# Optimization experiments

Hardware: AMD Instinct MI355X
Metric: run time of the kernel (lower is better)

The kernel has to match this reference:

```python
import jax, jax.numpy as jnp
import numpy as np

FREQ = 4
EXP_DIM = 32
INTERP_LEVEL = 3
DEFORM_SCALE = 0.1
BBOX = ((0.0, 1.0), (0.0, 1.0), (0.0, 1.0))
B, N = 2, 262144


def embed(x):
    # positional embedding: [x, sin(2^k x), cos(2^k x)] k=0..FREQ-1 (include_input, log sampling)
    feats = [x]
    for k in range(FREQ):
        s = x * (2.0 ** k)
        feats.append(jnp.sin(s))
        feats.append(jnp.cos(s))
    return jnp.concatenate(feats, axis=-1)


def mlp(x, W1, b1, W2, b2):
    return jax.nn.relu(x @ W1 + b1) @ W2 + b2


def grid_sample3d(vol, grid):
    # vol [C,D,H,W], grid [N,3] with (x,y,z) in [-1,1]; trilinear, align_corners=False, zero padding
    C, D, H, W = vol.shape
    fx = ((grid[:, 0] + 1.0) * W - 1.0) * 0.5
    fy = ((grid[:, 1] + 1.0) * H - 1.0) * 0.5
    fz = ((grid[:, 2] + 1.0) * D - 1.0) * 0.5
    x0 = jnp.floor(fx); y0 = jnp.floor(fy); z0 = jnp.floor(fz)
    wx = fx - x0; wy = fy - y0; wz = fz - z0
    x0i = x0.astype(jnp.int32); y0i = y0.astype(jnp.int32); z0i = z0.astype(jnp.int32)

    def gather(zi, yi, xi):
        valid = ((zi >= 0) & (zi < D) & (yi >= 0) & (yi < H) & (xi >= 0) & (xi < W))
        zc = jnp.clip(zi, 0, D - 1); yc = jnp.clip(yi, 0, H - 1); xc = jnp.clip(xi, 0, W - 1)
        return vol[:, zc, yc, xc] * valid.astype(vol.dtype)[None, :]

    out = jnp.zeros((C, grid.shape[0]), vol.dtype)
    for dz in (0, 1):
        for dy in (0, 1):
            for dx in (0, 1):
                w = ((wz if dz else 1.0 - wz) * (wy if dy else 1.0 - wy) * (wx if dx else 1.0 - wx))
                out = out + gather(z0i + dz, y0i + dy, x0i + dx) * w[None, :]
    return out


def normalize_pts(pts, bbox):
    # pts [B,3,N] -> grid [B,N,3] in [-1,1]
    uvw = []
    for i in range(3):
        lo, hi = bbox[i]
        uvw.append((pts[:, i] - 0.5 * (lo + hi)) / (0.5 * (hi - lo)))
    return jnp.stack(uvw, axis=-1)


def mult_dist_interp(pts, vol, bbox):
    # pts [B,3,N], vol [B,C,D,H,W] -> [B, C*INTERP_LEVEL, N]
    grid = normalize_pts(pts, bbox)
    feats = []
    for i in range(INTERP_LEVEL):
        s = 2 ** i
        sub = vol[:, :, ::s, ::s, ::s]
        feats.append(jax.vmap(grid_sample3d)(sub, grid))
    return jnp.concatenate(feats, axis=1)


def bcn_to_nc(x):
    b, c, n = x.shape
    return x.transpose(0, 2, 1).reshape(b * n, c)


def nc_to_bcn(x, b):
    bn, c = x.shape
    return x.reshape(b, bn // b, c).transpose(0, 2, 1)


def setup_inputs() -> dict:
    key = jax.random.key(0)
    ks = jax.random.split(key, 20)
    d = {
        'query_pts': jax.random.uniform(ks[0], (B, 3, N), jnp.float32),
        'query_viewdirs': jax.random.normal(ks[1], (B, 3, N), jnp.float32),
        'exp': jax.random.normal(ks[2], (B, 32), jnp.float32),
        'deform_bs_volume': jax.random.normal(ks[3], (32, 4, 32, 32, 32), jnp.float32) * 0.1,
        'deform_mean_volume': jax.random.normal(ks[4], (4, 32, 32, 32), jnp.float32) * 0.1,
        'feature_volume': jax.random.normal(ks[5], (8, 64, 64, 64), jnp.float32) * 0.1,
        'dW1': jax.random.normal(ks[6], (108, 64), jnp.float32) * 0.1,
        'db1': jnp.zeros((64,), jnp.float32),
        'dW2': jax.random.normal(ks[7], (64, 3), jnp.float32) * 0.1,
        'db2': jnp.zeros((3,), jnp.float32),
        'sW1': jax.random.normal(ks[8], (248, 128), jnp.float32) * 0.06,
        'sb1': jnp.zeros((128,), jnp.float32),
        'sW2': jax.random.normal(ks[9], (128, 1), jnp.float32) * 0.1,
        'sb2': jnp.zeros((1,), jnp.float32),
        'cW1': jax.random.normal(ks[10], (275, 128), jnp.float32) * 0.06,
        'cb1': jnp.zeros((128,), jnp.float32),
        'cW2': jax.random.normal(ks[11], (128, 3), jnp.float32) * 0.1,
        'cb2': jnp.zeros((3,), jnp.float32),
    }
    return d


def reference(query_pts, query_viewdirs, exp, deform_bs_volume, deform_mean_volume,
              feature_volume, dW1, db1, dW2, db2, sW1, sb1, sW2, sb2, cW1, cb1, cW2, cb2):
    b = query_pts.shape[0]
    exp_c = exp[:, :EXP_DIM]
    # deform volume: exp-blendshape combination  [B, Cd, R, R, R]
    deform_vol = jnp.einsum('be,ecdhw->bcdhw', exp_c, deform_bs_volume) + deform_mean_volume[None]
    deform = mult_dist_interp(query_pts, deform_vol, BBOX)            # [B, 12, N]
    offset = nc_to_bcn(mlp(embed(bcn_to_nc(deform)), dW1, db1, dW2, db2), b)  # [B,3,N]
    deformed_pts = offset * DEFORM_SCALE + query_pts
    fvol = jnp.broadcast_to(feature_volume[None], (b,) + feature_volume.shape)
    feature = mult_dist_interp(deformed_pts, fvol, BBOX)              # [B, 24, N]
    fe = embed(bcn_to_nc(feature))                                    # [(B N), 216]
    ve = embed(bcn_to_nc(query_viewdirs))                             # [(B N), 27]
    n = query_pts.shape[2]
    exp_n = jnp.broadcast_to((exp_c / 3.0)[:, None, :], (b, n, EXP_DIM)).reshape(b * n, EXP_DIM)
    density = nc_to_bcn(mlp(jnp.concatenate([fe, exp_n], 1), sW1, sb1, sW2, sb2), b)  # [B,1,N]
    color = jax.nn.sigmoid(nc_to_bcn(mlp(jnp.concatenate([fe, ve, exp_n], 1), cW1, cb1, cW2, cb2), b))  # [B,3,N]
    return offset, density, color
```

## Files before the change

### kernel.cpp

```cpp
#include <hip/hip_runtime.h>
#include <math.h>

#define NPTS 262144
#define RSTR 66

typedef __attribute__((ext_vector_type(4))) float f32x4;
typedef __attribute__((ext_vector_type(8))) short s16x8;

__device__ __forceinline__ unsigned short f2bf(float f) {
    union { float f; unsigned u; } v; v.f = f;
    unsigned u = v.u;
    return (unsigned short)((u + 0x7fffu + ((u >> 16) & 1u)) >> 16);
}
__device__ __forceinline__ float bf2f(unsigned short h) {
    union { unsigned u; float f; } v; v.u = ((unsigned)h) << 16;
    return v.f;
}
__device__ __forceinline__ unsigned rnd16(float f) {
    union { float f; unsigned u; } v; v.f = f;
    return v.u + 0x7fffu + ((v.u >> 16) & 1u);
}
__device__ __forceinline__ unsigned packbf(float lo, float hi) {
#if defined(__has_builtin)
#if __has_builtin(__builtin_amdgcn_perm)
    return __builtin_amdgcn_perm(rnd16(hi), rnd16(lo), 0x07060302u);
#else
    return (rnd16(hi) & 0xffff0000u) | (rnd16(lo) >> 16);
#endif
#else
    return (rnd16(hi) & 0xffff0000u) | (rnd16(lo) >> 16);
#endif
}

__device__ __forceinline__ int swz(int e) {
    return e ^ (((e >> 7) & 1) << 3) ^ (((e >> 8) & 1) << 4);
}

__device__ __forceinline__ int XF(int kt, int mt, int lane) {
    return ((kt * 4 + mt) * 64 + lane) * 8;
}

__device__ __forceinline__ int fragAddr(int p, int k) {
    int kt = k >> 5, kk = k & 31;
    int lane = (((kk & 15) >> 2) << 4) | (p & 15);
    int j = ((kk >> 4) << 2) | (kk & 3);
    int mt = (p >> 4) & 3;
    return swz((((kt * 4 + mt) * 64) + lane) * 8 + j);
}

__global__ void k_deform_vol_t(const float* __restrict__ exp_,
                               const float* __restrict__ bs,
                               const float* __restrict__ mean,
                               float* __restrict__ dvt) {
    int idx = blockIdx.x * blockDim.x + threadIdx.x;
    int c = idx & 3;
    int v = (idx >> 2) & 32767;
    int b = idx >> 17;
    float acc = mean[c * 32768 + v];
    #pragma unroll 8
    for (int e = 0; e < 32; ++e)
        acc = fmaf(exp_[b * 32 + e], bs[(e * 4 + c) * 32768 + v], acc);
    dvt[idx] = acc;
}

__global__ void k_ftr(const float* __restrict__ fvol, float* __restrict__ fvt) {
    int i = blockIdx.x * blockDim.x + threadIdx.x;
    int c = i >> 18;
    int v = i & 262143;
    fvt[v * 8 + c] = fvol[i];
}

__global__ void k_hb(const float* __restrict__ exp_,
                     const float* __restrict__ sW1, const float* __restrict__ sb1,
                     const float* __restrict__ cW1, const float* __restrict__ cb1,
                     float* __restrict__ sHb, float* __restrict__ cHb) {
    int b = blockIdx.x;
    int j = threadIdx.x;
    float a = sb1[j];
    float a2 = cb1[j];
    for (int e = 0; e < 32; ++e) {
        float ev = exp_[b * 32 + e] * (1.0f / 3.0f);
        a  = fmaf(ev, sW1[(216 + e) * 128 + j], a);
        a2 = fmaf(ev, cW1[(243 + e) * 128 + j], a2);
    }
    sHb[b * 128 + j] = a;
    cHb[b * 128 + j] = a2;
}

__global__ void k_wprep(const float* __restrict__ src,
                        unsigned short* __restrict__ dhi,
                        unsigned short* __restrict__ dlo,
                        int KT, int Nsrc, int Ksrc, int mode, int total) {
    int i = blockIdx.x * 256 + threadIdx.x;
    if (i >= total) return;
    int j = i & 7, lane = (i >> 3) & 63;
    int tile = i >> 9;
    int kt = tile % KT, nt = tile / KT;
    int n = nt * 16 + (lane & 15);
    int k = kt * 32 + ((lane >> 4) << 2) + (j & 3) + ((j >> 2) << 4);
    int row = -1;
    if (mode == 0) {
        row = (k < Ksrc) ? k : -1;
    } else if (mode == 1) {
        int g = k >> 5, tg = (k >> 4) & 1, r = k & 15;
        if (r < 12) row = 12 + 24 * g + 12 * tg + r;
        else { int idx = (2 * g + tg) * 4 + (r - 12); row = (idx < 12) ? idx : -1; }
    } else {
        int g = k >> 6, tg = (k >> 5) & 1, r = k & 31;
        if (r < 24) row = 24 + 48 * g + 24 * tg + r;
        else if (r < 27) row = (mode == 3) ? 219 + 6 * g + 3 * tg + (r - 24) : -1;
        else {
            int idx = (2 * g + tg) * 5 + (r - 27);
            if (idx < 24) row = idx;
            else if (idx < 27 && mode == 3) row = 216 + (idx - 24);
            else row = -1;
        }
    }
    float v = (row >= 0 && n < Nsrc) ? src[row * Nsrc + n] : 0.0f;
    unsigned short h = f2bf(v);
    dhi[i] = h;
    if (dlo) dlo[i] = f2bf(v - bf2f(h));
}

template<int S, int STEP, int DIM, int NC>
__device__ __forceinline__ void lerp_cl(const float* __restrict__ vol,
                                        float px, float py, float pz,
                                        float* __restrict__ o) {
    float fx = px * (float)S - 0.5f;
    float fy = py * (float)S - 0.5f;
    float fz = pz * (float)S - 0.5f;
    float x0 = floorf(fx), y0 = floorf(fy), z0 = floorf(fz);
    float wx = fx - x0, wy = fy - y0, wz = fz - z0;
    int ix = (int)x0, iy = (int)y0, iz = (int)z0;
    #pragma unroll
    for (int c = 0; c < NC; ++c) o[c] = 0.0f;
    #pragma unroll
    for (int dz = 0; dz < 2; ++dz)
    #pragma unroll
    for (int dy = 0; dy < 2; ++dy)
    #pragma unroll
    for (int dx = 0; dx < 2; ++dx) {
        int xi = ix + dx, yi = iy + dy, zi = iz + dz;
        bool valid = (xi >= 0) & (xi < S) & (yi >= 0) & (yi < S) & (zi >= 0) & (zi < S);
        int xc = min(max(xi, 0), S - 1);
        int yc = min(max(yi, 0), S - 1);
        int zc = min(max(zi, 0), S - 1);
        float w = (dz ? wz : 1.f - wz) * (dy ? wy : 1.f - wy) * (dx ? wx : 1.f - wx);
        w = valid ? w : 0.f;
        const float4* q = (const float4*)(vol +
            (size_t)(((zc * STEP) * DIM + yc * STEP) * DIM + xc * STEP) * NC);
        float4 v0 = q[0];
        o[0] = fmaf(v0.x, w, o[0]); o[1] = fmaf(v0.y, w, o[1]);
        o[2] = fmaf(v0.z, w, o[2]); o[3] = fmaf(v0.w, w, o[3]);
        if (NC == 8) {
            float4 v1 = q[1];
            o[4] = fmaf(v1.x, w, o[4]); o[5] = fmaf(v1.y, w, o[5]);
            o[6] = fmaf(v1.z, w, o[6]); o[7] = fmaf(v1.w, w, o[7]);
        }
    }
}

template<int C, int BD, int S, int STEP>
__device__ __forceinline__ void trilerp_cm(const float* __restrict__ vol,
                                           float px, float py, float pz,
                                           float* __restrict__ out) {
    float fx = px * (float)S - 0.5f;
    float fy = py * (float)S - 0.5f;
    float fz = pz * (float)S - 0.5f;
    float x0 = floorf(fx), y0 = floorf(fy), z0 = floorf(fz);
    float wx = fx - x0, wy = fy - y0, wz = fz - z0;
    int ix = (int)x0, iy = (int)y0, iz = (int)z0;
    #pragma unroll
    for (int c = 0; c < C; ++c) out[c] = 0.0f;
    #pragma unroll
    for (int dz = 0; dz < 2; ++dz)
    #pragma unroll
    for (int dy = 0; dy < 2; ++dy)
    #pragma unroll
    for (int dx = 0; dx < 2; ++dx) {
        int xi = ix + dx, yi = iy + dy, zi = iz + dz;
        bool valid = (xi >= 0) & (xi < S) & (yi >= 0) & (yi < S) & (zi >= 0) & (zi < S);
        int xc = min(max(xi, 0), S - 1);
        int yc = min(max(yi, 0), S - 1);
        int zc = min(max(zi, 0), S - 1);
        float w = (dz ? wz : 1.f - wz) * (dy ? wy : 1.f - wy) * (dx ? wx : 1.f - wx);
        w = valid ? w : 0.f;
        int off = ((zc * STEP) * BD + yc * STEP) * BD + xc * STEP;
        #pragma unroll
        for (int c = 0; c < C; ++c)
            out[c] = fmaf(vol[c * (BD * BD * BD) + off], w, out[c]);
    }
}

#define MFMA(a, b, c) __builtin_amdgcn_mfma_f32_16x16x32_bf16((a), (b), (c), 0, 0, 0)

template<bool CL>
__global__ __launch_bounds__(256, 4) void k_main(
    const float* __restrict__ qp, const float* __restrict__ qv,
    const float* __restrict__ dvt, const float* __restrict__ fvol,
    const float* __restrict__ db1, const float* __restrict__ db2,
    const float* __restrict__ sb2, const float* __restrict__ cb2,
    const float* __restrict__ sHb, const float* __restrict__ cHb,
    const unsigned short* __restrict__ dW1h, const unsigned short* __restrict__ dW1l,
    const unsigned short* __restrict__ sW1h,
    const unsigned short* __restrict__ cW1f,
    const unsigned short* __restrict__ dW2f, const unsigned short* __restrict__ sW2f,
    const unsigned short* __restrict__ cW2f,
    float* __restrict__ out)
{
    __shared__ __align__(16) unsigned short xfrag[16384];
    __shared__ __align__(16) float raw[28 * RSTR];
    __shared__ float dp[3 * 64];

    const int t = threadIdx.x;
    const int lane = t & 63;
    const int w = t >> 6;
    const int gp0 = blockIdx.x * 64;
    const int b = gp0 / NPTS;
    const int n0 = gp0 - b * NPTS;
    const float* qpb = qp + b * 3 * NPTS;
    const float* qvb = qv + b * 3 * NPTS;

    const int cc = (lane >> 4) << 2;
    const int pp = w * 16 + (lane & 15);

    {
        const float* dv = dvt + b * 131072;
        if (t < 192) {
            int p = t & 63, lvl = t >> 6;
            int n = n0 + p;
            float px = qpb[n], py = qpb[NPTS + n], pz = qpb[2 * NPTS + n];
            float o[4];
            if (lvl == 0)      lerp_cl<32, 1, 32, 4>(dv, px, py, pz, o);
            else if (lvl == 1) lerp_cl<16, 2, 32, 4>(dv, px, py, pz, o);
            else               lerp_cl< 8, 4, 32, 4>(dv, px, py, pz, o);
            #pragma unroll
            for (int c = 0; c < 4; ++c) raw[(lvl * 4 + c) * RSTR + p] = o[c];
        }
        if (t < 64) raw[12 * RSTR + t] = 0.f;
    }
    __syncthreads();

    {
        float s0[4], c0[4];
        #pragma unroll
        for (int m = 0; m < 4; ++m) {
            float x = raw[min(cc + m, 12) * RSTR + pp];
            s0[m] = __sinf(x);
            c0[m] = __cosf(x);
        }
        #pragma unroll
        for (int g = 0; g < 4; ++g) {
            float vs[8];
            #pragma unroll
            for (int m = 0; m < 4; ++m) {
                int r = cc + m;
                bool lad = r < 12;
                int i0 = (2 * g) * 4 + (r - 12);
                int i1 = (2 * g + 1) * 4 + (r - 12);
                float r0 = raw[min(max(i0, 0), 12) * RSTR + pp];
                float r1 = raw[min(max(i1, 0), 12) * RSTR + pp];
                vs[m]     = lad ? s0[m] : r0;
                vs[4 + m] = lad ? c0[m] : r1;
            }
            union { unsigned u[4]; s16x8 v; } pk;
            pk.u[0] = packbf(vs[0], vs[1]);
            pk.u[1] = packbf(vs[2], vs[3]);
            pk.u[2] = packbf(vs[4], vs[5]);
            pk.u[3] = packbf(vs[6], vs[7]);
            *(s16x8*)&xfrag[swz(XF(g, w, lane))] = pk.v;
            if (g < 3) {
                #pragma unroll
                for (int m = 0; m < 4; ++m) {
                    float s2 = 2.f * s0[m] * c0[m];
                    float c2 = c0[m] * c0[m] - s0[m] * s0[m];
                    s0[m] = s2; c0[m] = c2;
                }
            }
        }
    }
    __syncthreads();

    {
        f32x4 acc[4];
        float bias = db1[w * 16 + (lane & 15)];
        #pragma unroll
        for (int mt = 0; mt < 4; ++mt) acc[mt] = (f32x4){bias, bias, bias, bias};
        #pragma unroll 1
        for (int kt = 0; kt < 4; ++kt) {
            s16x8 bh = *(const s16x8*)&dW1h[((w * 4 + kt) * 64 + lane) * 8];
            s16x8 bl = *(const s16x8*)&dW1l[((w * 4 + kt) * 64 + lane) * 8];
            #pragma unroll
            for (int mt = 0; mt < 4; ++mt) {
                s16x8 a = *(const s16x8*)&xfrag[swz(XF(kt, mt, lane))];
                acc[mt] = MFMA(a, bh, acc[mt]);
                acc[mt] = MFMA(a, bl, acc[mt]);
            }
        }
        int j = w * 16 + (lane & 15);
        #pragma unroll
        for (int mt = 0; mt < 4; ++mt) {
            int a0 = fragAddr(mt * 16 + cc, 128 + j);
            #pragma unroll
            for (int i = 0; i < 4; ++i)
                xfrag[a0 ^ (8 * i)] = f2bf(fmaxf(acc[mt][i], 0.f));
        }
    }
    __syncthreads();

    {
        f32x4 acc = (f32x4){0, 0, 0, 0};
        #pragma unroll
        for (int kt = 0; kt < 2; ++kt) {
            s16x8 bb = *(const s16x8*)&dW2f[(kt * 64 + lane) * 8];
            s16x8 a = *(const s16x8*)&xfrag[swz(XF(4 + kt, w, lane))];
            acc = MFMA(a, bb, acc);
        }
        int col = lane & 15;
        if (col < 3) {
            #pragma unroll
            for (int i = 0; i < 4; ++i) {
                int p = w * 16 + ((lane >> 4) << 2) + i;
                float v = acc[i] + db2[col];
                out[(b * 3 + col) * NPTS + n0 + p] = v;
                dp[col * 64 + p] = fmaf(v, 0.1f, qpb[col * NPTS + n0 + p]);
            }
        }
    }
    __syncthreads();

    {
        if (t < 192) {
            int p = t & 63, lvl = t >> 6;
            float px = dp[p], py = dp[64 + p], pz = dp[128 + p];
            float o[8];
            if (CL) {
                if (lvl == 0)      lerp_cl<64, 1, 64, 8>(fvol, px, py, pz, o);
                else if (lvl == 1) lerp_cl<32, 2, 64, 8>(fvol, px, py, pz, o);
                else               lerp_cl<16, 4, 64, 8>(fvol, px, py, pz, o);
            } else {
                if (lvl == 0)      trilerp_cm<8, 64, 64, 1>(fvol, px, py, pz, o);
                else if (lvl == 1) trilerp_cm<8, 64, 32, 2>(fvol, px, py, pz, o);
                else               trilerp_cm<8, 64, 16, 4>(fvol, px, py, pz, o);
            }
            #pragma unroll
            for (int c = 0; c < 8; ++c) raw[(lvl * 8 + c) * RSTR + p] = o[c];
        }
        if (t < 64) {
            int n = n0 + t;
            raw[24 * RSTR + t] = qvb[n];
            raw[25 * RSTR + t] = qvb[NPTS + n];
            raw[26 * RSTR + t] = qvb[2 * NPTS + n];
            raw[27 * RSTR + t] = 0.f;
        }
    }
    __syncthreads();

    {
        float sL[4], cL[4], sH[4], cH[4];
        #pragma unroll
        for (int m = 0; m < 4; ++m) {
            float xl = raw[(cc + m) * RSTR + pp];
            sL[m] = __sinf(xl); cL[m] = __cosf(xl);
            float xh = raw[min(16 + cc + m, 27) * RSTR + pp];
            sH[m] = __sinf(xh); cH[m] = __cosf(xh);
        }
        #pragma unroll
        for (int g = 0; g < 4; ++g) {
            #pragma unroll
            for (int tg = 0; tg < 2; ++tg) {
                float vs[8];
                #pragma unroll
                for (int m = 0; m < 4; ++m) {
                    vs[m] = tg ? cL[m] : sL[m];
                    int rh = 16 + cc + m;
                    int idx = (2 * g + tg) * 5 + (rh - 27);
                    float rsv = raw[min(max(idx, 0), 27) * RSTR + pp];
                    float lad = tg ? cH[m] : sH[m];
                    vs[4 + m] = (rh < 27) ? lad : rsv;
                }
                union { unsigned u[4]; s16x8 v; } pk;
                pk.u[0] = packbf(vs[0], vs[1]);
                pk.u[1] = packbf(vs[2], vs[3]);
                pk.u[2] = packbf(vs[4], vs[5]);
                pk.u[3] = packbf(vs[6], vs[7]);
                *(s16x8*)&xfrag[swz(XF(2 * g + tg, w, lane))] = pk.v;
            }
            if (g < 3) {
                #pragma unroll
                for (int m = 0; m < 4; ++m) {
                    float s2 = 2.f * sL[m] * cL[m];
                    float c2 = cL[m] * cL[m] - sL[m] * sL[m];
                    sL[m] = s2; cL[m] = c2;
                    float s3 = 2.f * sH[m] * cH[m];
                    float c3 = cH[m] * cH[m] - sH[m] * sH[m];
                    sH[m] = s3; cH[m] = c3;
                }
            }
        }
    }
    __syncthreads();

    f32x4 accs[4][2], accc[4][2];
    {
        int nl = lane & 15;
        #pragma unroll
        for (int q = 0; q < 2; ++q) {
            float bsv = sHb[b * 128 + (2 * w + q) * 16 + nl];
            float bcv = cHb[b * 128 + (2 * w + q) * 16 + nl];
            #pragma unroll
            for (int mt = 0; mt < 4; ++mt) {
                accs[mt][q] = (f32x4){bsv, bsv, bsv, bsv};
                accc[mt][q] = (f32x4){bcv, bcv, bcv, bcv};
            }
        }
        #pragma unroll 1
        for (int kt = 0; kt < 8; ++kt) {
            s16x8 bh0 = *(const s16x8*)&sW1h[(((2 * w    ) * 8 + kt) * 64 + lane) * 8];
            s16x8 bh1 = *(const s16x8*)&sW1h[(((2 * w + 1) * 8 + kt) * 64 + lane) * 8];
            #pragma unroll
            for (int mt = 0; mt < 4; ++mt) {
                s16x8 a = *(const s16x8*)&xfrag[swz(XF(kt, mt, lane))];
                accs[mt][0] = MFMA(a, bh0, accs[mt][0]);
                accs[mt][1] = MFMA(a, bh1, accs[mt][1]);
            }
        }
        #pragma unroll 1
        for (int kt = 0; kt < 8; ++kt) {
            s16x8 b0 = *(const s16x8*)&cW1f[(((2 * w    ) * 8 + kt) * 64 + lane) * 8];
            s16x8 b1 = *(const s16x8*)&cW1f[(((2 * w + 1) * 8 + kt) * 64 + lane) * 8];
            #pragma unroll
            for (int mt = 0; mt < 4; ++mt) {
                s16x8 a = *(const s16x8*)&xfrag[swz(XF(kt, mt, lane))];
                accc[mt][0] = MFMA(a, b0, accc[mt][0]);
                accc[mt][1] = MFMA(a, b1, accc[mt][1]);
            }
        }
    }
    __syncthreads();

    {
        #pragma unroll
        for (int q = 0; q < 2; ++q) {
            int j = (2 * w + q) * 16 + (lane & 15);
            #pragma unroll
            for (int mt = 0; mt < 4; ++mt) {
                int a0 = fragAddr(mt * 16 + cc, j);
                #pragma unroll
                for (int i = 0; i < 4; ++i) {
                    int ai = a0 ^ (8 * i);
                    xfrag[ai]        = f2bf(fmaxf(accs[mt][q][i], 0.f));
                    xfrag[ai + 8192] = f2bf(fmaxf(accc[mt][q][i], 0.f));
                }
            }
        }
    }
    __syncthreads();

    {
        f32x4 as = (f32x4){0, 0, 0, 0};
        f32x4 ac = (f32x4){0, 0, 0, 0};
        #pragma unroll
        for (int kt = 0; kt < 4; ++kt) {
            s16x8 bsv = *(const s16x8*)&sW2f[(kt * 64 + lane) * 8];
            s16x8 bcv = *(const s16x8*)&cW2f[(kt * 64 + lane) * 8];
            s16x8 a1 = *(const s16x8*)&xfrag[swz(XF(kt, w, lane))];
            s16x8 a2 = *(const s16x8*)&xfrag[swz(XF(4 + kt, w, lane))];
            as = MFMA(a1, bsv, as);
            ac = MFMA(a2, bcv, ac);
        }
        int col = lane & 15;
        #pragma unroll
        for (int i = 0; i < 4; ++i) {
            int p = w * 16 + ((lane >> 4) << 2) + i;
            if (col == 0)
                out[6 * NPTS + b * NPTS + n0 + p] = as[i] + sb2[0];
            if (col < 3) {
                float v = ac[i] + cb2[col];
                out[8 * NPTS + (b * 3 + col) * NPTS + n0 + p] =
                    1.f / (1.f + __expf(-v));
            }
        }
    }
}

extern "C" void kernel_launch(void* const* d_in, const int* in_sizes, int n_in,
                              void* d_out, int out_size, void* d_ws, size_t ws_size,
                              hipStream_t stream) {
    const float* qp   = (const float*)d_in[0];
    const float* qv   = (const float*)d_in[1];
    const float* exp_ = (const float*)d_in[2];
    const float* bs   = (const float*)d_in[3];
    const float* mean = (const float*)d_in[4];
    const float* fvol = (const float*)d_in[5];
    const float* dW1  = (const float*)d_in[6];
    const float* db1  = (const float*)d_in[7];
    const float* dW2  = (const float*)d_in[8];
    const float* db2  = (const float*)d_in[9];
    const float* sW1  = (const float*)d_in[10];
    const float* sb1  = (const float*)d_in[11];
    const float* sW2  = (const float*)d_in[12];
    const float* sb2  = (const float*)d_in[13];
    const float* cW1  = (const float*)d_in[14];
    const float* cb1  = (const float*)d_in[15];
    const float* cW2  = (const float*)d_in[16];
    const float* cb2  = (const float*)d_in[17];

    float* out = (float*)d_out;
    float* ws  = (float*)d_ws;

    float* dvt = ws;
    float* sHb = ws + 262144;
    float* cHb = ws + 262400;
    unsigned short* wb = (unsigned short*)(ws + 262656);
    unsigned short* dW1h  = wb;
    unsigned short* dW1l  = wb + 8192;
    unsigned short* sW1h  = wb + 16384;
    unsigned short* cW1f_ = wb + 49152;
    unsigned short* dW2f  = wb + 81920;
    unsigned short* sW2f  = wb + 82944;
    unsigned short* cW2f  = wb + 84992;
    float* fvt = ws + 262656 + 43520;
    bool cl = ws_size >= (size_t)(306176 + 2097152) * 4;

    k_deform_vol_t<<<1024, 256, 0, stream>>>(exp_, bs, mean, dvt);
    k_hb<<<2, 128, 0, stream>>>(exp_, sW1, sb1, cW1, cb1, sHb, cHb);
    k_wprep<<<32, 256, 0, stream>>>(dW1, dW1h, dW1l, 4, 64, 128, 1, 8192);
    k_wprep<<<128, 256, 0, stream>>>(sW1, sW1h, nullptr, 8, 128, 256, 2, 32768);
    k_wprep<<<128, 256, 0, stream>>>(cW1, cW1f_, nullptr, 8, 128, 256, 3, 32768);
    k_wprep<<<4, 256, 0, stream>>>(dW2, dW2f, nullptr, 2, 3, 64, 0, 1024);
    k_wprep<<<8, 256, 0, stream>>>(sW2, sW2f, nullptr, 4, 1, 128, 0, 2048);
    k_wprep<<<8, 256, 0, stream>>>(cW2, cW2f, nullptr, 4, 3, 128, 0, 2048);

    if (cl) {
        k_ftr<<<2097152 / 256, 256, 0, stream>>>(fvol, fvt);
        k_main<true><<<8192, 256, 0, stream>>>(
            qp, qv, dvt, fvt, db1, db2, sb2, cb2, sHb, cHb,
            dW1h, dW1l, sW1h, cW1f_, dW2f, sW2f, cW2f, out);
    } else {
        k_main<false><<<8192, 256, 0, stream>>>(
            qp, qv, dvt, fvol, db1, db2, sb2, cb2, sHb, cHb,
            dW1h, dW1l, sW1h, cW1f_, dW2f, sW2f, cW2f, out);
    }
}
```

Before: 253.4 us.

## Make each wave own 16 points end-to-end and replace block barriers with wave waits

Reassigns work so each wavefront processes its own 16 points through all stages. Lanes are split by level for the trilinear sampling, and each wave computes all output columns of every MLP GEMM for its M-tile instead of splitting columns across waves. Since no wave reads another wave's LDS data, all __syncthreads are replaced by an lgkmcnt wait with scheduling barriers, removing block-wide barrier stalls. In exchange each wave loads every weight fragment from global/L2, which raises weight traffic fourfold, and the sampling template now takes runtime sizes and shifts instead of compile-time constants.

```diff
diff --git a/kernel.cpp b/kernel.cpp
--- a/kernel.cpp
+++ b/kernel.cpp
@@ -30,6 +30,12 @@
 #else
     return (rnd16(hi) & 0xffff0000u) | (rnd16(lo) >> 16);
 #endif
+}
+
+__device__ __forceinline__ void wave_sync() {
+    __builtin_amdgcn_sched_barrier(0);
+    asm volatile("s_waitcnt lgkmcnt(0)" ::: "memory");
+    __builtin_amdgcn_sched_barrier(0);
 }
 
 __device__ __forceinline__ int swz(int e) {
@@ -122,13 +128,15 @@
     if (dlo) dlo[i] = f2bf(v - bf2f(h));
 }
 
-template<int S, int STEP, int DIM, int NC>
-__device__ __forceinline__ void lerp_cl(const float* __restrict__ vol,
-                                        float px, float py, float pz,
-                                        float* __restrict__ o) {
-    float fx = px * (float)S - 0.5f;
-    float fy = py * (float)S - 0.5f;
-    float fz = pz * (float)S - 0.5f;
+template<int DIM, int NC>
+__device__ __forceinline__ void lerp_cl_rt(const float* __restrict__ vol,
+                                           int S, int lc,
+                                           float px, float py, float pz,
+                                           float* __restrict__ o) {
+    float fS = (float)S;
+    float fx = px * fS - 0.5f;
+    float fy = py * fS - 0.5f;
+    float fz = pz * fS - 0.5f;
     float x0 = floorf(fx), y0 = floorf(fy), z0 = floorf(fz);
     float wx = fx - x0, wy = fy - y0, wz = fz - z0;
     int ix = (int)x0, iy = (int)y0, iz = (int)z0;
@@ -145,33 +153,35 @@
         int xc = min(max(xi, 0), S - 1);
         int yc = min(max(yi, 0), S - 1);
         int zc = min(max(zi, 0), S - 1);
-        float w = (dz ? wz : 1.f - wz) * (dy ? wy : 1.f - wy) * (dx ? wx : 1.f - wx);
-        w = valid ? w : 0.f;
+        float wgt = (dz ? wz : 1.f - wz) * (dy ? wy : 1.f - wy) * (dx ? wx : 1.f - wx);
+        wgt = valid ? wgt : 0.f;
         const float4* q = (const float4*)(vol +
-            (size_t)(((zc * STEP) * DIM + yc * STEP) * DIM + xc * STEP) * NC);
+            (size_t)(((zc << lc) * DIM + (yc << lc)) * DIM + (xc << lc)) * NC);
         float4 v0 = q[0];
-        o[0] = fmaf(v0.x, w, o[0]); o[1] = fmaf(v0.y, w, o[1]);
-        o[2] = fmaf(v0.z, w, o[2]); o[3] = fmaf(v0.w, w, o[3]);
+        o[0] = fmaf(v0.x, wgt, o[0]); o[1] = fmaf(v0.y, wgt, o[1]);
+        o[2] = fmaf(v0.z, wgt, o[2]); o[3] = fmaf(v0.w, wgt, o[3]);
         if (NC == 8) {
             float4 v1 = q[1];
-            o[4] = fmaf(v1.x, w, o[4]); o[5] = fmaf(v1.y, w, o[5]);
-            o[6] = fmaf(v1.z, w, o[6]); o[7] = fmaf(v1.w, w, o[7]);
-        }
-    }
-}
-
-template<int C, int BD, int S, int STEP>
-__device__ __forceinline__ void trilerp_cm(const float* __restrict__ vol,
+            o[4] = fmaf(v1.x, wgt, o[4]); o[5] = fmaf(v1.y, wgt, o[5]);
+            o[6] = fmaf(v1.z, wgt, o[6]); o[7] = fmaf(v1.w, wgt, o[7]);
+        }
+    }
+}
+
+template<int DIM, int NC>
+__device__ __forceinline__ void lerp_cm_rt(const float* __restrict__ vol,
+                                           int S, int lc,
                                            float px, float py, float pz,
-                                           float* __restrict__ out) {
-    float fx = px * (float)S - 0.5f;
-    float fy = py * (float)S - 0.5f;
-    float fz = pz * (float)S - 0.5f;
+                                           float* __restrict__ o) {
+    float fS = (float)S;
+    float fx = px * fS - 0.5f;
+    float fy = py * fS - 0.5f;
+    float fz = pz * fS - 0.5f;
     float x0 = floorf(fx), y0 = floorf(fy), z0 = floorf(fz);
     float wx = fx - x0, wy = fy - y0, wz = fz - z0;
     int ix = (int)x0, iy = (int)y0, iz = (int)z0;
     #pragma unroll
-    for (int c = 0; c < C; ++c) out[c] = 0.0f;
+    for (int c = 0; c < NC; ++c) o[c] = 0.0f;
     #pragma unroll
     for (int dz = 0; dz < 2; ++dz)
     #pragma unroll
@@ -183,12 +193,12 @@
         int xc = min(max(xi, 0), S - 1);
         int yc = min(max(yi, 0), S - 1);
         int zc = min(max(zi, 0), S - 1);
-        float w = (dz ? wz : 1.f - wz) * (dy ? wy : 1.f - wy) * (dx ? wx : 1.f - wx);
-        w = valid ? w : 0.f;
-        int off = ((zc * STEP) * BD + yc * STEP) * BD + xc * STEP;
-        #pragma unroll
-        for (int c = 0; c < C; ++c)
-            out[c] = fmaf(vol[c * (BD * BD * BD) + off], w, out[c]);
+        float wgt = (dz ? wz : 1.f - wz) * (dy ? wy : 1.f - wy) * (dx ? wx : 1.f - wx);
+        wgt = valid ? wgt : 0.f;
+        int off = ((zc << lc) * DIM + (yc << lc)) * DIM + (xc << lc);
+        #pragma unroll
+        for (int c = 0; c < NC; ++c)
+            o[c] = fmaf(vol[c * (DIM * DIM * DIM) + off], wgt, o[c]);
     }
 }
 
@@ -222,24 +232,26 @@
     const float* qvb = qv + b * 3 * NPTS;
 
     const int cc = (lane >> 4) << 2;
-    const int pp = w * 16 + (lane & 15);
+    const int nl = lane & 15;
+    const int pp = w * 16 + nl;
+    const int pl = lane & 15;
+    const int lvl = lane >> 4;
+    const int pg = w * 16 + pl;
 
     {
         const float* dv = dvt + b * 131072;
-        if (t < 192) {
-            int p = t & 63, lvl = t >> 6;
-            int n = n0 + p;
+        if (lvl < 3) {
+            int n = n0 + pg;
             float px = qpb[n], py = qpb[NPTS + n], pz = qpb[2 * NPTS + n];
             float o[4];
-            if (lvl == 0)      lerp_cl<32, 1, 32, 4>(dv, px, py, pz, o);
-            else if (lvl == 1) lerp_cl<16, 2, 32, 4>(dv, px, py, pz, o);
-            else               lerp_cl< 8, 4, 32, 4>(dv, px, py, pz, o);
-            #pragma unroll
-            for (int c = 0; c < 4; ++c) raw[(lvl * 4 + c) * RSTR + p] = o[c];
-        }
-        if (t < 64) raw[12 * RSTR + t] = 0.f;
-    }
-    __syncthreads();
+            lerp_cl_rt<32, 4>(dv, 32 >> lvl, lvl, px, py, pz, o);
+            #pragma unroll
+            for (int c = 0; c < 4; ++c) raw[(lvl * 4 + c) * RSTR + pg] = o[c];
+        } else {
+            raw[12 * RSTR + pg] = 0.f;
+        }
+    }
+    wave_sync();
 
     {
         float s0[4], c0[4];
@@ -279,34 +291,36 @@
             }
         }
     }
-    __syncthreads();
+    wave_sync();
 
     {
         f32x4 acc[4];
-        float bias = db1[w * 16 + (lane & 15)];
-        #pragma unroll
-        for (int mt = 0; mt < 4; ++mt) acc[mt] = (f32x4){bias, bias, bias, bias};
+        #pragma unroll
+        for (int nt = 0; nt < 4; ++nt) {
+            float bias = db1[nt * 16 + nl];
+            acc[nt] = (f32x4){bias, bias, bias, bias};
+        }
         #pragma unroll 1
         for (int kt = 0; kt < 4; ++kt) {
-            s16x8 bh = *(const s16x8*)&dW1h[((w * 4 + kt) * 64 + lane) * 8];
-            s16x8 bl = *(const s16x8*)&dW1l[((w * 4 + kt) * 64 + lane) * 8];
-            #pragma unroll
-            for (int mt = 0; mt < 4; ++mt) {
-                s16x8 a = *(const s16x8*)&xfrag[swz(XF(kt, mt, lane))];
-                acc[mt] = MFMA(a, bh, acc[mt]);
-                acc[mt] = MFMA(a, bl, acc[mt]);
-            }
-        }
-        int j = w * 16 + (lane & 15);
-        #pragma unroll
-        for (int mt = 0; mt < 4; ++mt) {
-            int a0 = fragAddr(mt * 16 + cc, 128 + j);
+            s16x8 a = *(const s16x8*)&xfrag[swz(XF(kt, w, lane))];
+            #pragma unroll
+            for (int nt = 0; nt < 4; ++nt) {
+                s16x8 bh = *(const s16x8*)&dW1h[((nt * 4 + kt) * 64 + lane) * 8];
+                s16x8 bl = *(const s16x8*)&dW1l[((nt * 4 + kt) * 64 + lane) * 8];
+                acc[nt] = MFMA(a, bh, acc[nt]);
+                acc[nt] = MFMA(a, bl, acc[nt]);
+            }
+        }
+        wave_sync();
+        #pragma unroll
+        for (int nt = 0; nt < 4; ++nt) {
+            int a0 = fragAddr(w * 16 + cc, 128 + nt * 16 + nl);
             #pragma unroll
             for (int i = 0; i < 4; ++i)
-                xfrag[a0 ^ (8 * i)] = f2bf(fmaxf(acc[mt][i], 0.f));
-        }
-    }
-    __syncthreads();
+                xfrag[a0 ^ (8 * i)] = f2bf(fmaxf(acc[nt][i], 0.f));
+        }
+    }
+    wave_sync();
 
     {
         f32x4 acc = (f32x4){0, 0, 0, 0};
@@ -320,41 +334,32 @@
         if (col < 3) {
             #pragma unroll
             for (int i = 0; i < 4; ++i) {
-                int p = w * 16 + ((lane >> 4) << 2) + i;
+                int p = w * 16 + cc + i;
                 float v = acc[i] + db2[col];
                 out[(b * 3 + col) * NPTS + n0 + p] = v;
                 dp[col * 64 + p] = fmaf(v, 0.1f, qpb[col * NPTS + n0 + p]);
             }
         }
     }
-    __syncthreads();
-
-    {
-        if (t < 192) {
-            int p = t & 63, lvl = t >> 6;
-            float px = dp[p], py = dp[64 + p], pz = dp[128 + p];
+    wave_sync();
+
+    {
+        if (lvl < 3) {
+            float px = dp[pg], py = dp[64 + pg], pz = dp[128 + pg];
             float o[8];
-            if (CL) {
-                if (lvl == 0)      lerp_cl<64, 1, 64, 8>(fvol, px, py, pz, o);
-                else if (lvl == 1) lerp_cl<32, 2, 64, 8>(fvol, px, py, pz, o);
-                else               lerp_cl<16, 4, 64, 8>(fvol, px, py, pz, o);
-            } else {
-                if (lvl == 0)      trilerp_cm<8, 64, 64, 1>(fvol, px, py, pz, o);
-                else if (lvl == 1) trilerp_cm<8, 64, 32, 2>(fvol, px, py, pz, o);
-                else               trilerp_cm<8, 64, 16, 4>(fvol, px, py, pz, o);
-            }
-            #pragma unroll
-            for (int c = 0; c < 8; ++c) raw[(lvl * 8 + c) * RSTR + p] = o[c];
-        }
-        if (t < 64) {
-            int n = n0 + t;
-            raw[24 * RSTR + t] = qvb[n];
-            raw[25 * RSTR + t] = qvb[NPTS + n];
-            raw[26 * RSTR + t] = qvb[2 * NPTS + n];
-            raw[27 * RSTR + t] = 0.f;
-        }
-    }
-    __syncthreads();
+            if (CL) lerp_cl_rt<64, 8>(fvol, 64 >> lvl, lvl, px, py, pz, o);
+            else    lerp_cm_rt<64, 8>(fvol, 64 >> lvl, lvl, px, py, pz, o);
+            #pragma unroll
+            for (int c = 0; c < 8; ++c) raw[(lvl * 8 + c) * RSTR + pg] = o[c];
+        } else {
+            int n = n0 + pg;
+            raw[24 * RSTR + pg] = qvb[n];
+            raw[25 * RSTR + pg] = qvb[NPTS + n];
+            raw[26 * RSTR + pg] = qvb[2 * NPTS + n];
+            raw[27 * RSTR + pg] = 0.f;
+        }
+    }
+    wave_sync();
 
     {
         float sL[4], cL[4], sH[4], cH[4];
@@ -399,63 +404,47 @@
             }
         }
     }
-    __syncthreads();
-
-    f32x4 accs[4][2], accc[4][2];
-    {
-        int nl = lane & 15;
-        #pragma unroll
-        for (int q = 0; q < 2; ++q) {
-            float bsv = sHb[b * 128 + (2 * w + q) * 16 + nl];
-            float bcv = cHb[b * 128 + (2 * w + q) * 16 + nl];
-            #pragma unroll
-            for (int mt = 0; mt < 4; ++mt) {
-                accs[mt][q] = (f32x4){bsv, bsv, bsv, bsv};
-                accc[mt][q] = (f32x4){bcv, bcv, bcv, bcv};
-            }
+    wave_sync();
+
+    f32x4 accs[8], accc[8];
+    {
+        #pragma unroll
+        for (int nt = 0; nt < 8; ++nt) {
+            float bsv = sHb[b * 128 + nt * 16 + nl];
+            float bcv = cHb[b * 128 + nt * 16 + nl];
+            accs[nt] = (f32x4){bsv, bsv, bsv, bsv};
+            accc[nt] = (f32x4){bcv, bcv, bcv, bcv};
         }
         #pragma unroll 1
         for (int kt = 0; kt < 8; ++kt) {
-            s16x8 bh0 = *(const s16x8*)&sW1h[(((2 * w    ) * 8 + kt) * 64 + lane) * 8];
-            s16x8 bh1 = *(const s16x8*)&sW1h[(((2 * w + 1) * 8 + kt) * 64 + lane) * 8];
-            #pragma unroll
-            for (int mt = 0; mt < 4; ++mt) {
-                s16x8 a = *(const s16x8*)&xfrag[swz(XF(kt, mt, lane))];
-                accs[mt][0] = MFMA(a, bh0, accs[mt][0]);
-                accs[mt][1] = MFMA(a, bh1, accs[mt][1]);
-            }
-        }
-        #pragma unroll 1
-        for (int kt = 0; kt < 8; ++kt) {
-            s16x8 b0 = *(const s16x8*)&cW1f[(((2 * w    ) * 8 + kt) * 64 + lane) * 8];
-            s16x8 b1 = *(const s16x8*)&cW1f[(((2 * w + 1) * 8 + kt) * 64 + lane) * 8];
-            #pragma unroll
-            for (int mt = 0; mt < 4; ++mt) {
-                s16x8 a = *(const s16x8*)&xfrag[swz(XF(kt, mt, lane))];
-                accc[mt][0] = MFMA(a, b0, accc[mt][0]);
-                accc[mt][1] = MFMA(a, b1, accc[mt][1]);
-            }
-        }
-    }
-    __syncthreads();
-
-    {
-        #pragma unroll
-        for (int q = 0; q < 2; ++q) {
-            int j = (2 * w + q) * 16 + (lane & 15);
-            #pragma unroll
-            for (int mt = 0; mt < 4; ++mt) {
-                int a0 = fragAddr(mt * 16 + cc, j);
-                #pragma unroll
-                for (int i = 0; i < 4; ++i) {
-                    int ai = a0 ^ (8 * i);
-                    xfrag[ai]        = f2bf(fmaxf(accs[mt][q][i], 0.f));
-                    xfrag[ai + 8192] = f2bf(fmaxf(accc[mt][q][i], 0.f));
-                }
-            }
-        }
-    }
-    __syncthreads();
+            s16x8 a = *(const s16x8*)&xfrag[swz(XF(kt, w, lane))];
+            #pragma unroll
+            for (int nt = 0; nt < 8; ++nt) {
+                s16x8 bs = *(const s16x8*)&sW1h[((nt * 8 + kt) * 64 + lane) * 8];
+                accs[nt] = MFMA(a, bs, accs[nt]);
+            }
+            #pragma unroll
+            for (int nt = 0; nt < 8; ++nt) {
+                s16x8 bc = *(const s16x8*)&cW1f[((nt * 8 + kt) * 64 + lane) * 8];
+                accc[nt] = MFMA(a, bc, accc[nt]);
+            }
+        }
+    }
+    wave_sync();
+
+    {
+        #pragma unroll
+        for (int nt = 0; nt < 8; ++nt) {
+            int a0 = fragAddr(w * 16 + cc, nt * 16 + nl);
+            #pragma unroll
+            for (int i = 0; i < 4; ++i) {
+                int ai = a0 ^ (8 * i);
+                xfrag[ai]        = f2bf(fmaxf(accs[nt][i], 0.f));
+                xfrag[ai + 8192] = f2bf(fmaxf(accc[nt][i], 0.f));
+            }
+        }
+    }
+    wave_sync();
 
     {
         f32x4 as = (f32x4){0, 0, 0, 0};
@@ -472,7 +461,7 @@
         int col = lane & 15;
         #pragma unroll
         for (int i = 0; i < 4; ++i) {
-            int p = w * 16 + ((lane >> 4) << 2) + i;
+            int p = w * 16 + cc + i;
             if (col == 0)
                 out[6 * NPTS + b * NPTS + n0 + p] = as[i] + sb2[0];
             if (col < 3) {
```

Measured after the change: 408.6 us. 61.3% more time.
